# Performance work log

Measured on AMD Instinct MI355X. Metric: run time of the kernel, lower is better.

Reference implementation:

```python
import jax, jax.numpy as jnp
import numpy as np

D = 1024
H = 16
HD = D // H
E = 64
K = 2


def setup_inputs() -> dict:
    key = jax.random.key(0)
    ks = jax.random.split(key, 10)
    s = 0.02
    return {
        "x": jax.random.normal(ks[0], (8, 2048, D), dtype=jnp.float32),
        "expert_embeddings": jax.random.normal(ks[1], (E, D), dtype=jnp.float32),
        "in_proj_w": jax.random.normal(ks[2], (3 * D, D), dtype=jnp.float32) * s,
        "in_proj_b": jax.random.normal(ks[3], (3 * D,), dtype=jnp.float32) * s,
        "out_proj_w": jax.random.normal(ks[4], (D, D), dtype=jnp.float32) * s,
        "out_proj_b": jax.random.normal(ks[5], (D,), dtype=jnp.float32) * s,
        "gate_w1": jax.random.normal(ks[6], (4 * E, D), dtype=jnp.float32) * s,
        "gate_b1": jax.random.normal(ks[7], (4 * E,), dtype=jnp.float32) * s,
        "gate_w2": jax.random.normal(ks[8], (E, 4 * E), dtype=jnp.float32) * s,
        "gate_b2": jax.random.normal(ks[9], (E,), dtype=jnp.float32) * s,
    }


def reference(x, expert_embeddings, in_proj_w, in_proj_b, out_proj_w, out_proj_b,
              gate_w1, gate_b1, gate_w2, gate_b2):
    B, S, _ = x.shape
    wq, wk, wv = jnp.split(in_proj_w, 3, axis=0)   # each (D, D)
    bq, bk, bv = jnp.split(in_proj_b, 3, axis=0)
    # cross-attention: queries from x, keys/values from expert embeddings (shared across batch)
    q = (x @ wq.T + bq).reshape(B, S, H, HD)                      # (B,S,H,hd)
    k = (expert_embeddings @ wk.T + bk).reshape(E, H, HD)         # (E,H,hd)
    v = (expert_embeddings @ wv.T + bv).reshape(E, H, HD)
    scores = jnp.einsum('bshd,ehd->bhse', q, k) / jnp.sqrt(jnp.float32(HD))
    attn = jax.nn.softmax(scores, axis=-1)                        # (B,H,S,E)
    o = jnp.einsum('bhse,ehd->bshd', attn, v).reshape(B, S, D)
    attn_out = o @ out_proj_w.T + out_proj_b                      # (B,S,D)
    # gate MLP (exact GELU like torch default)
    h = jax.nn.gelu(attn_out @ gate_w1.T + gate_b1, approximate=False)
    gate_logits = h @ gate_w2.T + gate_b2                         # (B,S,E)
    probs = jax.nn.softmax(gate_logits, axis=-1)
    vals, idx = jax.lax.top_k(probs, K)                           # (B,S,K)
    weights = vals / (jnp.sum(vals, axis=-1, keepdims=True) + 1e-8)
    return idx, weights
```

## Files before the change

### kernel.cpp

```cpp
#include <hip/hip_runtime.h>
#include <math.h>


typedef _Float16 h8 __attribute__((ext_vector_type(8)));
typedef _Float16 h4 __attribute__((ext_vector_type(4)));
typedef float f4 __attribute__((ext_vector_type(4)));

__device__ __forceinline__ float gelu_exact(float x) {
    return 0.5f * x * (1.0f + erff(x * 0.70710678118654752f));
}

__global__ __launch_bounds__(256) void split2_kernel(
    const float* __restrict__ src, _Float16* __restrict__ dst, long total, int colsh) {
    long i = ((long)blockIdx.x * 256 + threadIdx.x) * 4;
    if (i >= total) return;
    f4 v = *(const f4*)(src + i);
    long row = i >> colsh; int col = (int)(i & ((1 << colsh) - 1));
    _Float16* d0 = dst + (row << (colsh + 1)) + col;
    h4 lo, hi;
    #pragma unroll
    for (int j = 0; j < 4; j++) {
        _Float16 a = (_Float16)v[j];
        lo[j] = a;
        hi[j] = (_Float16)((v[j] - (float)a) * 4096.0f);
    }
    *(h4*)d0 = lo;
    *(h4*)(d0 + (1 << colsh)) = hi;
}

__global__ __launch_bounds__(256) void kv_kernel(
    const float* __restrict__ w, const float* __restrict__ b,
    const float* __restrict__ ee, float* __restrict__ kbuf, float* __restrict__ vtbuf) {
    __shared__ float As[32][68];
    __shared__ float Bs[32][68];
    int tid = threadIdx.x;
    int r0 = blockIdx.x * 64;
    int tx = tid & 15, ty = tid >> 4;
    float acc[4][4] = {};
    const float* wbase = w + (size_t)(1024 + r0) * 1024;
    for (int k0 = 0; k0 < 1024; k0 += 32) {
        #pragma unroll
        for (int i = 0; i < 2; i++) {
            int f = tid + i * 256;
            int row = f >> 3, c4 = f & 7;
            float4 v = *(const float4*)(wbase + (size_t)row * 1024 + k0 + c4 * 4);
            As[c4*4+0][row] = v.x; As[c4*4+1][row] = v.y;
            As[c4*4+2][row] = v.z; As[c4*4+3][row] = v.w;
            float4 u = *(const float4*)(ee + (size_t)row * 1024 + k0 + c4 * 4);
            Bs[c4*4+0][row] = u.x; Bs[c4*4+1][row] = u.y;
            Bs[c4*4+2][row] = u.z; Bs[c4*4+3][row] = u.w;
        }
        __syncthreads();
        #pragma unroll
        for (int kk = 0; kk < 32; kk++) {
            float a[4], bb[4];
            *(float4*)&a[0]  = *(const float4*)&As[kk][ty * 4];
            *(float4*)&bb[0] = *(const float4*)&Bs[kk][tx * 4];
            #pragma unroll
            for (int i = 0; i < 4; i++)
                #pragma unroll
                for (int j = 0; j < 4; j++)
                    acc[i][j] = fmaf(a[i], bb[j], acc[i][j]);
        }
        __syncthreads();
    }
    #pragma unroll
    for (int i = 0; i < 4; i++) {
        int row = r0 + ty * 4 + i;
        float bias = b[1024 + row];
        int j = row & 1023;
        int h = j >> 6, hd = j & 63;
        #pragma unroll
        for (int jj = 0; jj < 4; jj++) {
            int e = tx * 4 + jj;
            float val = acc[i][jj] + bias;
            if (row < 1024) kbuf[h * 4096 + e * 64 + hd] = val;
            else            vtbuf[h * 4096 + hd * 64 + e] = val;
        }
    }
}

template<int GELU, int OSPLIT>
__global__ __launch_bounds__(256, 2) void hgemm_kernel(
    const _Float16* __restrict__ A, const _Float16* __restrict__ B,
    const float* __restrict__ bias, void* __restrict__ Cv, int ldc, int nhalf) {
    __shared__ __align__(16) _Float16 As[128 * 40];
    __shared__ __align__(16) _Float16 Bl[128 * 40];
    __shared__ __align__(16) _Float16 Bh[128 * 40];
    int tid = threadIdx.x;
    int m0 = blockIdx.y * 128, n0 = blockIdx.x * 128;
    int w = tid >> 6, l = tid & 63;
    int wm = w & 1, wn = w >> 1;
    int lr = l & 15, lk = l >> 4;

    f4 acc1[4][4], acc2[4][4];
    #pragma unroll
    for (int i = 0; i < 4; i++)
        #pragma unroll
        for (int j = 0; j < 4; j++) {
            acc1[i][j] = (f4){0.f, 0.f, 0.f, 0.f};
            acc2[i][j] = (f4){0.f, 0.f, 0.f, 0.f};
        }

    int f0 = tid, f1 = tid + 256;
    int r0 = f0 >> 2, c0 = f0 & 3, r1 = f1 >> 2, c1 = f1 & 3;
    int s0 = r0 * 40 + c0 * 8, s1 = r1 * 40 + c1 * 8;
    const _Float16* Ab = A + (size_t)m0 * 2048;
    const _Float16* Bb = B + (size_t)n0 * 2048;

    uint4 ua0, ua1, ub0, ub1, uc0, uc1;
    ua0 = *(const uint4*)(Ab + (size_t)r0 * 2048 + c0 * 8);
    ua1 = *(const uint4*)(Ab + (size_t)r1 * 2048 + c1 * 8);
    ub0 = *(const uint4*)(Bb + (size_t)r0 * 2048 + c0 * 8);
    ub1 = *(const uint4*)(Bb + (size_t)r1 * 2048 + c1 * 8);
    uc0 = *(const uint4*)(Bb + (size_t)r0 * 2048 + 1024 + c0 * 8);
    uc1 = *(const uint4*)(Bb + (size_t)r1 * 2048 + 1024 + c1 * 8);

    for (int kt = 0; kt < 32; kt++) {
        __syncthreads();
        *(uint4*)(As + s0) = ua0; *(uint4*)(As + s1) = ua1;
        *(uint4*)(Bl + s0) = ub0; *(uint4*)(Bl + s1) = ub1;
        *(uint4*)(Bh + s0) = uc0; *(uint4*)(Bh + s1) = uc1;
        __syncthreads();
        if (kt < 31) {
            int ka = (kt + 1) * 32;
            ua0 = *(const uint4*)(Ab + (size_t)r0 * 2048 + ka + c0 * 8);
            ua1 = *(const uint4*)(Ab + (size_t)r1 * 2048 + ka + c1 * 8);
            ub0 = *(const uint4*)(Bb + (size_t)r0 * 2048 + ka + c0 * 8);
            ub1 = *(const uint4*)(Bb + (size_t)r1 * 2048 + ka + c1 * 8);
            uc0 = *(const uint4*)(Bb + (size_t)r0 * 2048 + 1024 + ka + c0 * 8);
            uc1 = *(const uint4*)(Bb + (size_t)r1 * 2048 + 1024 + ka + c1 * 8);
        } else {
            ua0 = *(const uint4*)(Ab + (size_t)r0 * 2048 + 1024 + c0 * 8);
            ua1 = *(const uint4*)(Ab + (size_t)r1 * 2048 + 1024 + c1 * 8);
            uc0 = *(const uint4*)(Bb + (size_t)r0 * 2048 + c0 * 8);
            uc1 = *(const uint4*)(Bb + (size_t)r1 * 2048 + c1 * 8);
        }
        h8 af[4], blf[4], bhf[4];
        #pragma unroll
        for (int mi = 0; mi < 4; mi++)
            af[mi] = *(const h8*)(As + (wm * 64 + mi * 16 + lr) * 40 + lk * 8);
        #pragma unroll
        for (int ni = 0; ni < 4; ni++) {
            blf[ni] = *(const h8*)(Bl + (wn * 64 + ni * 16 + lr) * 40 + lk * 8);
            bhf[ni] = *(const h8*)(Bh + (wn * 64 + ni * 16 + lr) * 40 + lk * 8);
        }
        #pragma unroll
        for (int mi = 0; mi < 4; mi++)
            #pragma unroll
            for (int ni = 0; ni < 4; ni++) {
                acc1[mi][ni] = __builtin_amdgcn_mfma_f32_16x16x32_f16(af[mi], blf[ni], acc1[mi][ni], 0, 0, 0);
                acc2[mi][ni] = __builtin_amdgcn_mfma_f32_16x16x32_f16(af[mi], bhf[ni], acc2[mi][ni], 0, 0, 0);
            }
    }

    for (int kt = 0; kt < 32; kt++) {
        __syncthreads();
        *(uint4*)(As + s0) = ua0; *(uint4*)(As + s1) = ua1;
        *(uint4*)(Bh + s0) = uc0; *(uint4*)(Bh + s1) = uc1;
        __syncthreads();
        if (kt < 31) {
            int ka = (kt + 1) * 32;
            ua0 = *(const uint4*)(Ab + (size_t)r0 * 2048 + 1024 + ka + c0 * 8);
            ua1 = *(const uint4*)(Ab + (size_t)r1 * 2048 + 1024 + ka + c1 * 8);
            uc0 = *(const uint4*)(Bb + (size_t)r0 * 2048 + ka + c0 * 8);
            uc1 = *(const uint4*)(Bb + (size_t)r1 * 2048 + ka + c1 * 8);
        }
        h8 af[4], bhf[4];
        #pragma unroll
        for (int mi = 0; mi < 4; mi++)
            af[mi] = *(const h8*)(As + (wm * 64 + mi * 16 + lr) * 40 + lk * 8);
        #pragma unroll
        for (int ni = 0; ni < 4; ni++)
            bhf[ni] = *(const h8*)(Bh + (wn * 64 + ni * 16 + lr) * 40 + lk * 8);
        #pragma unroll
        for (int mi = 0; mi < 4; mi++)
            #pragma unroll
            for (int ni = 0; ni < 4; ni++)
                acc2[mi][ni] = __builtin_amdgcn_mfma_f32_16x16x32_f16(af[mi], bhf[ni], acc2[mi][ni], 0, 0, 0);
    }

    #pragma unroll
    for (int mi = 0; mi < 4; mi++)
        #pragma unroll
        for (int ni = 0; ni < 4; ni++) {
            int n = n0 + wn * 64 + ni * 16 + lr;
            float bn = bias[n];
            #pragma unroll
            for (int j = 0; j < 4; j++) {
                int m = m0 + wm * 64 + mi * 16 + lk * 4 + j;
                float val = acc1[mi][ni][j] + acc2[mi][ni][j] * (1.0f / 4096.0f) + bn;
                if (GELU) val = gelu_exact(val);
                if (OSPLIT) {
                    _Float16* Ch = (_Float16*)Cv;
                    _Float16 lo = (_Float16)val;
                    Ch[(size_t)m * ldc + n] = lo;
                    Ch[(size_t)m * ldc + nhalf + n] = (_Float16)((val - (float)lo) * 4096.0f);
                } else {
                    ((float*)Cv)[(size_t)m * ldc + n] = val;
                }
            }
        }
}

__global__ __launch_bounds__(256) void attn2_kernel(
    const float* __restrict__ kbuf, const float* __restrict__ vtbuf,
    const float* __restrict__ q, _Float16* __restrict__ os) {
    __shared__ __align__(16) float qs[4][64][68];
    __shared__ __align__(16) float ps[4][2][64];
    int tid = threadIdx.x;
    int w = tid >> 6, l = tid & 63;
    int wid = blockIdx.x * 4 + w;
    int b = wid >> 9, h = (wid >> 5) & 15, t0 = (wid & 31) * 64;

    f4 kr[16], vt[16];
    const f4* kp = (const f4*)(kbuf + h * 4096 + l * 64);
    const f4* vp = (const f4*)(vtbuf + h * 4096 + l * 64);
    #pragma unroll
    for (int i = 0; i < 16; i++) { kr[i] = kp[i]; vt[i] = vp[i]; }

    const float* qbase = q + ((size_t)(b * 2048 + t0)) * 1024 + h * 64;
    #pragma unroll
    for (int it = 0; it < 16; it++) {
        int f = it * 64 + l;
        int r = f >> 4, c = f & 15;
        f4 v = *(const f4*)(qbase + (size_t)r * 1024 + c * 4);
        *(f4*)&qs[w][r][c * 4] = v;
    }

    for (int t = 0; t < 64; t++) {
        float s = 0.f;
        #pragma unroll
        for (int i = 0; i < 16; i++) {
            f4 qv = *(const f4*)&qs[w][t][i * 4];
            s = fmaf(qv[0], kr[i][0], s);
            s = fmaf(qv[1], kr[i][1], s);
            s = fmaf(qv[2], kr[i][2], s);
            s = fmaf(qv[3], kr[i][3], s);
        }
        s *= 0.125f;
        float ex = __expf(s);
        float sum = ex;
        #pragma unroll
        for (int off = 32; off; off >>= 1) sum += __shfl_xor(sum, off, 64);
        float p = ex / sum;
        ps[w][t & 1][l] = p;
        float o = 0.f;
        #pragma unroll
        for (int i = 0; i < 16; i++) {
            f4 pv = *(const f4*)&ps[w][t & 1][i * 4];
            o = fmaf(pv[0], vt[i][0], o);
            o = fmaf(pv[1], vt[i][1], o);
            o = fmaf(pv[2], vt[i][2], o);
            o = fmaf(pv[3], vt[i][3], o);
        }
        _Float16 o1 = (_Float16)o;
        _Float16 o2 = (_Float16)((o - (float)o1) * 4096.0f);
        size_t tok = (size_t)(b * 2048 + t0 + t);
        os[tok * 2048 + h * 64 + l] = o1;
        os[tok * 2048 + 1024 + h * 64 + l] = o2;
    }
}

__global__ __launch_bounds__(256) void gate2_kernel(
    const _Float16* __restrict__ h1s, const _Float16* __restrict__ w2s,
    const float* __restrict__ b2, float* __restrict__ out) {
    int tid = threadIdx.x;
    int w = tid >> 6, l = tid & 63;
    int lr = l & 15, lk = l >> 4;
    int trow = blockIdx.x * 64 + w * 16;

    f4 acc1[4], acc2[4], acc3[4];
    #pragma unroll
    for (int ni = 0; ni < 4; ni++) {
        acc1[ni] = (f4){0.f,0.f,0.f,0.f};
        acc2[ni] = (f4){0.f,0.f,0.f,0.f};
        acc3[ni] = (f4){0.f,0.f,0.f,0.f};
    }
    const _Float16* Arow = h1s + (size_t)(trow + lr) * 512;
    #pragma unroll
    for (int kt = 0; kt < 8; kt++) {
        h8 a1 = *(const h8*)(Arow + kt * 32 + lk * 8);
        h8 a2 = *(const h8*)(Arow + 256 + kt * 32 + lk * 8);
        #pragma unroll
        for (int ni = 0; ni < 4; ni++) {
            const _Float16* Brow = w2s + (size_t)(ni * 16 + lr) * 512;
            h8 b1 = *(const h8*)(Brow + kt * 32 + lk * 8);
            h8 bh = *(const h8*)(Brow + 256 + kt * 32 + lk * 8);
            acc1[ni] = __builtin_amdgcn_mfma_f32_16x16x32_f16(a1, b1, acc1[ni], 0, 0, 0);
            acc2[ni] = __builtin_amdgcn_mfma_f32_16x16x32_f16(a1, bh, acc2[ni], 0, 0, 0);
            acc2[ni] = __builtin_amdgcn_mfma_f32_16x16x32_f16(a2, b1, acc2[ni], 0, 0, 0);
            acc3[ni] = __builtin_amdgcn_mfma_f32_16x16x32_f16(a2, bh, acc3[ni], 0, 0, 0);
        }
    }
    float bcol[4];
    #pragma unroll
    for (int ni = 0; ni < 4; ni++) bcol[ni] = b2[ni * 16 + lr];

    const float c1 = 1.0f / 4096.0f, c2 = 1.0f / 16777216.0f;
    #pragma unroll
    for (int j = 0; j < 4; j++) {
        int tok = trow + lk * 4 + j;
        float lg[4];
        #pragma unroll
        for (int ni = 0; ni < 4; ni++)
            lg[ni] = acc1[ni][j] + acc2[ni][j] * c1 + acc3[ni][j] * c2 + bcol[ni];
        float mx = fmaxf(fmaxf(lg[0], lg[1]), fmaxf(lg[2], lg[3]));
        #pragma unroll
        for (int off = 1; off <= 8; off <<= 1) mx = fmaxf(mx, __shfl_xor(mx, off, 64));
        float pr[4], s = 0.f;
        #pragma unroll
        for (int ni = 0; ni < 4; ni++) { pr[ni] = expf(lg[ni] - mx); s += pr[ni]; }
        #pragma unroll
        for (int off = 1; off <= 8; off <<= 1) s += __shfl_xor(s, off, 64);
        float inv = 1.0f / s;
        float v1 = -1.f, v2 = -1.f; int i1 = 0, i2 = 0;
        #pragma unroll
        for (int ni = 0; ni < 4; ni++) {
            float p = pr[ni] * inv;
            int e = ni * 16 + lr;
            if (p > v1) { v2 = v1; i2 = i1; v1 = p; i1 = e; }
            else if (p > v2) { v2 = p; i2 = e; }
        }
        #pragma unroll
        for (int off = 1; off <= 8; off <<= 1) {
            float u1 = __shfl_xor(v1, off, 64); int k1 = __shfl_xor(i1, off, 64);
            float u2 = __shfl_xor(v2, off, 64); int k2 = __shfl_xor(i2, off, 64);
            if (u1 > v1) {
                if (v1 > u2) { v2 = v1; i2 = i1; } else { v2 = u2; i2 = k2; }
                v1 = u1; i1 = k1;
            } else if (u1 > v2) { v2 = u1; i2 = k1; }
        }
        if (lr == 0) {
            float wsum = v1 + v2 + 1e-8f;
            out[(size_t)tok * 2]     = (float)i1;
            out[(size_t)tok * 2 + 1] = (float)i2;
            out[32768 + (size_t)tok * 2]     = v1 / wsum;
            out[32768 + (size_t)tok * 2 + 1] = v2 / wsum;
        }
    }
}

extern "C" void kernel_launch(void* const* d_in, const int* in_sizes, int n_in,
                              void* d_out, int out_size, void* d_ws, size_t ws_size,
                              hipStream_t stream) {
    const float* x   = (const float*)d_in[0];
    const float* ee  = (const float*)d_in[1];
    const float* ipw = (const float*)d_in[2];
    const float* ipb = (const float*)d_in[3];
    const float* opw = (const float*)d_in[4];
    const float* opb = (const float*)d_in[5];
    const float* gw1 = (const float*)d_in[6];
    const float* gb1 = (const float*)d_in[7];
    const float* gw2 = (const float*)d_in[8];
    const float* gb2 = (const float*)d_in[9];
    float* out = (float*)d_out;
    char* ws = (char*)d_ws;

    _Float16* xs    = (_Float16*)ws;
    _Float16* h1s   = (_Float16*)ws;
    float*    qbuf  = (float*)(ws + 67108864);
    _Float16* aos   = (_Float16*)(ws + 67108864);
    _Float16* wqs   = (_Float16*)(ws + 134217728);
    _Float16* opws  = (_Float16*)(ws + 138412032);
    _Float16* gw1s  = (_Float16*)(ws + 142606336);
    float*    kbuf  = (float*)(ws + 143654912);
    _Float16* gw2s  = (_Float16*)(ws + 143654912);
    float*    vtbuf = (float*)(ws + 143917056);

    split2_kernel<<<dim3(1024),  dim3(256), 0, stream>>>(ipw, wqs, 1048576L, 10);
    split2_kernel<<<dim3(1024),  dim3(256), 0, stream>>>(opw, opws, 1048576L, 10);
    split2_kernel<<<dim3(256),   dim3(256), 0, stream>>>(gw1, gw1s, 262144L, 10);
    split2_kernel<<<dim3(16384), dim3(256), 0, stream>>>(x, xs, 16777216L, 10);
    kv_kernel<<<dim3(32), dim3(256), 0, stream>>>(ipw, ipb, ee, kbuf, vtbuf);
    hgemm_kernel<0,0><<<dim3(8, 128), dim3(256), 0, stream>>>(xs, wqs, ipb, qbuf, 1024, 0);
    attn2_kernel<<<dim3(1024), dim3(256), 0, stream>>>(kbuf, vtbuf, qbuf, xs);
    split2_kernel<<<dim3(16), dim3(256), 0, stream>>>(gw2, gw2s, 16384L, 8);
    hgemm_kernel<0,1><<<dim3(8, 128), dim3(256), 0, stream>>>(xs, opws, opb, (void*)aos, 2048, 1024);
    hgemm_kernel<1,1><<<dim3(2, 128), dim3(256), 0, stream>>>(aos, gw1s, gb1, (void*)h1s, 512, 256);
    gate2_kernel<<<dim3(256), dim3(256), 0, stream>>>(h1s, gw2s, gb2, out);
}
```

Measured before the change: 649.3 us.

## Load GEMM tiles directly global-to-LDS and raise occupancy bound

The fp16 split-precision GEMM no longer stages the next tile in registers. It now uses global_load_lds to copy 16-byte chunks straight into shared memory on each k-step. The LDS row padding is removed (stride 40 to 32) to fit the direct-copy layout, and launch bounds go from 2 to 4 blocks per SIMD group so more waves can hide latency. The cost is the loss of explicit register prefetch overlap, possible LDS bank conflicts from the unpadded layout, and register pressure or spills from the 128 accumulator values under the tighter occupancy bound.

```diff
diff --git a/kernel.cpp b/kernel.cpp
--- a/kernel.cpp
+++ b/kernel.cpp
@@ -5,6 +5,10 @@
 typedef _Float16 h8 __attribute__((ext_vector_type(8)));
 typedef _Float16 h4 __attribute__((ext_vector_type(4)));
 typedef float f4 __attribute__((ext_vector_type(4)));
+
+#define GLOAD16(g, l) __builtin_amdgcn_global_load_lds( \
+    (const __attribute__((address_space(1))) unsigned int*)(g), \
+    (__attribute__((address_space(3))) unsigned int*)(l), 16, 0, 0)
 
 __device__ __forceinline__ float gelu_exact(float x) {
     return 0.5f * x * (1.0f + erff(x * 0.70710678118654752f));
@@ -81,12 +85,12 @@
 }
 
 template<int GELU, int OSPLIT>
-__global__ __launch_bounds__(256, 2) void hgemm_kernel(
+__global__ __launch_bounds__(256, 4) void hgemm_kernel(
     const _Float16* __restrict__ A, const _Float16* __restrict__ B,
     const float* __restrict__ bias, void* __restrict__ Cv, int ldc, int nhalf) {
-    __shared__ __align__(16) _Float16 As[128 * 40];
-    __shared__ __align__(16) _Float16 Bl[128 * 40];
-    __shared__ __align__(16) _Float16 Bh[128 * 40];
+    __shared__ __align__(16) _Float16 As[128 * 32];
+    __shared__ __align__(16) _Float16 Bl[128 * 32];
+    __shared__ __align__(16) _Float16 Bh[128 * 32];
     int tid = threadIdx.x;
     int m0 = blockIdx.y * 128, n0 = blockIdx.x * 128;
     int w = tid >> 6, l = tid & 63;
@@ -102,48 +106,32 @@
             acc2[i][j] = (f4){0.f, 0.f, 0.f, 0.f};
         }
 
-    int f0 = tid, f1 = tid + 256;
-    int r0 = f0 >> 2, c0 = f0 & 3, r1 = f1 >> 2, c1 = f1 & 3;
-    int s0 = r0 * 40 + c0 * 8, s1 = r1 * 40 + c1 * 8;
+    int r0 = tid >> 2, c0 = (tid & 3) * 8;
+    int r1 = r0 + 64;
     const _Float16* Ab = A + (size_t)m0 * 2048;
     const _Float16* Bb = B + (size_t)n0 * 2048;
-
-    uint4 ua0, ua1, ub0, ub1, uc0, uc1;
-    ua0 = *(const uint4*)(Ab + (size_t)r0 * 2048 + c0 * 8);
-    ua1 = *(const uint4*)(Ab + (size_t)r1 * 2048 + c1 * 8);
-    ub0 = *(const uint4*)(Bb + (size_t)r0 * 2048 + c0 * 8);
-    ub1 = *(const uint4*)(Bb + (size_t)r1 * 2048 + c1 * 8);
-    uc0 = *(const uint4*)(Bb + (size_t)r0 * 2048 + 1024 + c0 * 8);
-    uc1 = *(const uint4*)(Bb + (size_t)r1 * 2048 + 1024 + c1 * 8);
+    _Float16* As0 = As + tid * 8;  _Float16* As1 = As + (tid + 256) * 8;
+    _Float16* Bl0 = Bl + tid * 8;  _Float16* Bl1 = Bl + (tid + 256) * 8;
+    _Float16* Bh0 = Bh + tid * 8;  _Float16* Bh1 = Bh + (tid + 256) * 8;
 
     for (int kt = 0; kt < 32; kt++) {
-        __syncthreads();
-        *(uint4*)(As + s0) = ua0; *(uint4*)(As + s1) = ua1;
-        *(uint4*)(Bl + s0) = ub0; *(uint4*)(Bl + s1) = ub1;
-        *(uint4*)(Bh + s0) = uc0; *(uint4*)(Bh + s1) = uc1;
-        __syncthreads();
-        if (kt < 31) {
-            int ka = (kt + 1) * 32;
-            ua0 = *(const uint4*)(Ab + (size_t)r0 * 2048 + ka + c0 * 8);
-            ua1 = *(const uint4*)(Ab + (size_t)r1 * 2048 + ka + c1 * 8);
-            ub0 = *(const uint4*)(Bb + (size_t)r0 * 2048 + ka + c0 * 8);
-            ub1 = *(const uint4*)(Bb + (size_t)r1 * 2048 + ka + c1 * 8);
-            uc0 = *(const uint4*)(Bb + (size_t)r0 * 2048 + 1024 + ka + c0 * 8);
-            uc1 = *(const uint4*)(Bb + (size_t)r1 * 2048 + 1024 + ka + c1 * 8);
-        } else {
-            ua0 = *(const uint4*)(Ab + (size_t)r0 * 2048 + 1024 + c0 * 8);
-            ua1 = *(const uint4*)(Ab + (size_t)r1 * 2048 + 1024 + c1 * 8);
-            uc0 = *(const uint4*)(Bb + (size_t)r0 * 2048 + c0 * 8);
-            uc1 = *(const uint4*)(Bb + (size_t)r1 * 2048 + c1 * 8);
-        }
+        int ka = kt * 32;
+        __syncthreads();
+        GLOAD16(Ab + (size_t)r0 * 2048 + ka + c0, As0);
+        GLOAD16(Ab + (size_t)r1 * 2048 + ka + c0, As1);
+        GLOAD16(Bb + (size_t)r0 * 2048 + ka + c0, Bl0);
+        GLOAD16(Bb + (size_t)r1 * 2048 + ka + c0, Bl1);
+        GLOAD16(Bb + (size_t)r0 * 2048 + 1024 + ka + c0, Bh0);
+        GLOAD16(Bb + (size_t)r1 * 2048 + 1024 + ka + c0, Bh1);
+        __syncthreads();
         h8 af[4], blf[4], bhf[4];
         #pragma unroll
         for (int mi = 0; mi < 4; mi++)
-            af[mi] = *(const h8*)(As + (wm * 64 + mi * 16 + lr) * 40 + lk * 8);
+            af[mi] = *(const h8*)(As + (wm * 64 + mi * 16 + lr) * 32 + lk * 8);
         #pragma unroll
         for (int ni = 0; ni < 4; ni++) {
-            blf[ni] = *(const h8*)(Bl + (wn * 64 + ni * 16 + lr) * 40 + lk * 8);
-            bhf[ni] = *(const h8*)(Bh + (wn * 64 + ni * 16 + lr) * 40 + lk * 8);
+            blf[ni] = *(const h8*)(Bl + (wn * 64 + ni * 16 + lr) * 32 + lk * 8);
+            bhf[ni] = *(const h8*)(Bh + (wn * 64 + ni * 16 + lr) * 32 + lk * 8);
         }
         #pragma unroll
         for (int mi = 0; mi < 4; mi++)
@@ -155,24 +143,20 @@
     }
 
     for (int kt = 0; kt < 32; kt++) {
-        __syncthreads();
-        *(uint4*)(As + s0) = ua0; *(uint4*)(As + s1) = ua1;
-        *(uint4*)(Bh + s0) = uc0; *(uint4*)(Bh + s1) = uc1;
-        __syncthreads();
-        if (kt < 31) {
-            int ka = (kt + 1) * 32;
-            ua0 = *(const uint4*)(Ab + (size_t)r0 * 2048 + 1024 + ka + c0 * 8);
-            ua1 = *(const uint4*)(Ab + (size_t)r1 * 2048 + 1024 + ka + c1 * 8);
-            uc0 = *(const uint4*)(Bb + (size_t)r0 * 2048 + ka + c0 * 8);
-            uc1 = *(const uint4*)(Bb + (size_t)r1 * 2048 + ka + c1 * 8);
-        }
+        int ka = kt * 32;
+        __syncthreads();
+        GLOAD16(Ab + (size_t)r0 * 2048 + 1024 + ka + c0, As0);
+        GLOAD16(Ab + (size_t)r1 * 2048 + 1024 + ka + c0, As1);
+        GLOAD16(Bb + (size_t)r0 * 2048 + ka + c0, Bh0);
+        GLOAD16(Bb + (size_t)r1 * 2048 + ka + c0, Bh1);
+        __syncthreads();
         h8 af[4], bhf[4];
         #pragma unroll
         for (int mi = 0; mi < 4; mi++)
-            af[mi] = *(const h8*)(As + (wm * 64 + mi * 16 + lr) * 40 + lk * 8);
+            af[mi] = *(const h8*)(As + (wm * 64 + mi * 16 + lr) * 32 + lk * 8);
         #pragma unroll
         for (int ni = 0; ni < 4; ni++)
-            bhf[ni] = *(const h8*)(Bh + (wn * 64 + ni * 16 + lr) * 40 + lk * 8);
+            bhf[ni] = *(const h8*)(Bh + (wn * 64 + ni * 16 + lr) * 32 + lk * 8);
         #pragma unroll
         for (int mi = 0; mi < 4; mi++)
             #pragma unroll
```

Result: slower. 2.012 ms (+209.8%).
